# Performance work log

Hardware: AMD Instinct MI355X
Metric: run time of the kernel (lower is better)

The kernel has to match this reference:

```python
import jax, jax.numpy as jnp
import numpy as np

B, L, D, H, NB = 32, 200, 512, 8, 2
HD = D // H
EPS = 1e-8


def _ln(x, g, b):
    m = x.mean(-1, keepdims=True)
    v = ((x - m) ** 2).mean(-1, keepdims=True)
    return (x - m) / jnp.sqrt(v + EPS) * g + b


def setup_inputs() -> dict:
    key = jax.random.key(0)
    ks = jax.random.split(key, 12)
    w = lambda k, shape: (jax.random.normal(k, shape, jnp.float32) * 0.02)
    return {
        "x": jax.random.normal(ks[0], (B, L, D), jnp.float32),
        "timeline_mask": jnp.zeros((B, L), dtype=bool),  # True = padded
        "ln1_g": jnp.ones((NB, D), jnp.float32), "ln1_b": jnp.zeros((NB, D), jnp.float32),
        "Wq": w(ks[1], (NB, D, D)), "bq": jnp.zeros((NB, D), jnp.float32),
        "Wk": w(ks[2], (NB, D, D)), "bk": jnp.zeros((NB, D), jnp.float32),
        "Wv": w(ks[3], (NB, D, D)), "bv": jnp.zeros((NB, D), jnp.float32),
        "Wo": w(ks[4], (NB, D, D)), "bo": jnp.zeros((NB, D), jnp.float32),
        "ln2_g": jnp.ones((NB, D), jnp.float32), "ln2_b": jnp.zeros((NB, D), jnp.float32),
        "W1": w(ks[5], (NB, D, D)), "b1": jnp.zeros((NB, D), jnp.float32),
        "W2": w(ks[6], (NB, D, D)), "b2": jnp.zeros((NB, D), jnp.float32),
        "lnf_g": jnp.ones((D,), jnp.float32), "lnf_b": jnp.zeros((D,), jnp.float32),
    }


def reference(x, timeline_mask, ln1_g, ln1_b, Wq, bq, Wk, bk, Wv, bv, Wo, bo,
              ln2_g, ln2_b, W1, b1, W2, b2, lnf_g, lnf_b):
    valid = (~timeline_mask)[..., None].astype(x.dtype)  # [B,L,1]
    # causal additive bias [L,L]: 0 on/below diag, -inf above
    causal = jnp.where(jnp.tril(jnp.ones((L, L), dtype=bool)), 0.0, -jnp.inf).astype(x.dtype)
    scale = 1.0 / (HD ** 0.5)
    q = x * valid  # dropout = identity (eval)
    for i in range(NB):
        Qn = _ln(q, ln1_g[i], ln1_b[i])  # pre-attn LayerNorm (query side)
        qh = (Qn @ Wq[i] + bq[i]).reshape(B, L, H, HD)
        kh = (q @ Wk[i] + bk[i]).reshape(B, L, H, HD)
        vh = (q @ Wv[i] + bv[i]).reshape(B, L, H, HD)
        scores = jnp.einsum('bqhd,bkhd->bhqk', qh, kh) * scale + causal
        attn = jax.nn.softmax(scores, axis=-1)
        ctx = jnp.einsum('bhqk,bkhd->bqhd', attn, vh).reshape(B, L, D)
        q = ctx @ Wo[i] + bo[i] + Qn          # residual to normed Q (as in source)
        q = _ln(q, ln2_g[i], ln2_b[i])        # forward layernorm
        h = jax.nn.relu(q @ W1[i] + b1[i]) @ W2[i] + b2[i]  # 1x1 convs == per-token MLP
        q = (q + h) * valid                   # PWFF residual, then timeline mask
    return _ln(q, lnf_g, lnf_b)
```

## Files before the change

kernel.cpp:

```cpp
#include <hip/hip_runtime.h>

typedef unsigned short u16;
typedef __bf16 bfloat;
typedef bfloat bf16x8 __attribute__((ext_vector_type(8)));
typedef float f32x4 __attribute__((ext_vector_type(4)));
typedef u16 v8u16 __attribute__((ext_vector_type(8)));
typedef u16 v4u16 __attribute__((ext_vector_type(4)));

#define B_ 32
#define L_ 200
#define D_ 512
#define H_ 8
#define HD_ 64
#define M_ (B_*L_)

__device__ __forceinline__ float bf2f(u16 u) {
  union { float f; unsigned int i; } v; v.i = ((unsigned int)u) << 16; return v.f;
}
__device__ __forceinline__ u16 f2bf(float f) {
  union { float f; unsigned int i; } v; v.f = f;
  unsigned int i = v.i;
  return (u16)((i + 0x7FFFu + ((i >> 16) & 1u)) >> 16);
}
__device__ __forceinline__ bf16x8 as_bf(v8u16 v) { return __builtin_bit_cast(bf16x8, v); }

__device__ __forceinline__ void gload16(const void* g, void* l) {
  __builtin_amdgcn_global_load_lds(
      (const __attribute__((address_space(1))) void*)g,
      (__attribute__((address_space(3))) void*)l,
      16, 0, 0);
}

struct TPtrs { const float* s[12]; };

__global__ __launch_bounds__(256) void prep_kernel(
    const float* __restrict__ x, const unsigned char* __restrict__ mask,
    u16* __restrict__ qb, TPtrs tp, u16* __restrict__ dst)
{
  __shared__ float T[64][65];
  int bid = blockIdx.x;
  int t = threadIdx.x;
  if (bid < 1600) {
    size_t i = (size_t)bid * 256 + t;
    size_t base = i * 8;
    int tok = (int)(base >> 9);
    float valid = mask[tok] ? 0.f : 1.f;
    float4 v0 = *(const float4*)(x + base);
    float4 v1 = *(const float4*)(x + base + 4);
    v8u16 ob;
    ob[0]=f2bf(v0.x*valid); ob[1]=f2bf(v0.y*valid); ob[2]=f2bf(v0.z*valid); ob[3]=f2bf(v0.w*valid);
    ob[4]=f2bf(v1.x*valid); ob[5]=f2bf(v1.y*valid); ob[6]=f2bf(v1.z*valid); ob[7]=f2bf(v1.w*valid);
    *(v8u16*)(qb + base) = ob;
  } else {
    int wb   = bid - 1600;
    int mat  = wb >> 6;
    int tile = wb & 63;
    int tr = tile >> 3, tc = tile & 7;
    const float* src = tp.s[mat];
    #pragma unroll
    for (int i = 0; i < 4; i++) {
      int idx = t + i * 256;
      int row = idx >> 4, c4 = idx & 15;
      float4 v = *(const float4*)(src + (size_t)(tr * 64 + row) * 512 + tc * 64 + c4 * 4);
      T[row][c4 * 4 + 0] = v.x; T[row][c4 * 4 + 1] = v.y;
      T[row][c4 * 4 + 2] = v.z; T[row][c4 * 4 + 3] = v.w;
    }
    __syncthreads();
    u16* d = dst + (size_t)mat * 262144;
    #pragma unroll
    for (int i = 0; i < 2; i++) {
      int idx = t + i * 256;
      int row = idx >> 3, c8 = idx & 7;
      v8u16 v;
      #pragma unroll
      for (int j = 0; j < 8; j++) v[j] = f2bf(T[c8 * 8 + j][row]);
      *(v8u16*)(d + (size_t)(tc * 64 + row) * 512 + tr * 64 + c8 * 8) = v;
    }
  }
}

template<bool OUTF32>
__global__ __launch_bounds__(256) void ln_kernel(
    const u16* __restrict__ in, const float* __restrict__ g, const float* __restrict__ b,
    u16* __restrict__ outb, float* __restrict__ outf)
{
  int row  = blockIdx.x * 4 + (threadIdx.x >> 6);
  int lane = threadIdx.x & 63;
  size_t base = (size_t)row * 512 + lane * 8;
  v8u16 xv = *(const v8u16*)(in + base);
  float xs[8];
  #pragma unroll
  for (int j = 0; j < 8; j++) xs[j] = bf2f(xv[j]);
  float s = 0.f, q = 0.f;
  #pragma unroll
  for (int j = 0; j < 8; j++) { s += xs[j]; q += xs[j] * xs[j]; }
  #pragma unroll
  for (int off = 1; off < 64; off <<= 1) { s += __shfl_xor(s, off); q += __shfl_xor(q, off); }
  float mean = s * (1.f / 512.f);
  float var  = fmaxf(q * (1.f / 512.f) - mean * mean, 0.f);
  float rstd = rsqrtf(var + 1e-8f);
  float4 g0 = *(const float4*)(g + lane * 8);
  float4 g1 = *(const float4*)(g + lane * 8 + 4);
  float4 b0 = *(const float4*)(b + lane * 8);
  float4 b1 = *(const float4*)(b + lane * 8 + 4);
  float gv[8] = {g0.x,g0.y,g0.z,g0.w,g1.x,g1.y,g1.z,g1.w};
  float bv[8] = {b0.x,b0.y,b0.z,b0.w,b1.x,b1.y,b1.z,b1.w};
  if (OUTF32) {
    float of[8];
    #pragma unroll
    for (int j = 0; j < 8; j++) of[j] = (xs[j] - mean) * rstd * gv[j] + bv[j];
    *(float4*)(outf + base)     = make_float4(of[0], of[1], of[2], of[3]);
    *(float4*)(outf + base + 4) = make_float4(of[4], of[5], of[6], of[7]);
  } else {
    v8u16 ob;
    #pragma unroll
    for (int j = 0; j < 8; j++) ob[j] = f2bf((xs[j] - mean) * rstd * gv[j] + bv[j]);
    *(v8u16*)(outb + base) = ob;
  }
}

__device__ __forceinline__ void gemm_core(
    const u16* __restrict__ A, const u16* __restrict__ Wt,
    int m0, int n0, u16* As, u16* Bs, f32x4 (&acc)[2][4])
{
  int tid = threadIdx.x, wid = tid >> 6, lane = tid & 63;
  int wr = wid >> 1, wc = wid & 1;
  int l15 = lane & 15, hi = lane >> 4;
  int sr8 = lane >> 3;
  int gsw = (lane & 7) ^ sr8;

  for (int s = 0; s < 8; s++) {
    int kk = s * 64;
    #pragma unroll
    for (int i = 0; i < 2; i++) {
      int rb = i * 32 + wid * 8;
      gload16(A + (size_t)(m0 + rb + sr8) * 512 + kk + gsw * 8, (char*)As + rb * 128);
    }
    #pragma unroll
    for (int j = 0; j < 4; j++) {
      int rb = j * 32 + wid * 8;
      gload16(Wt + (size_t)(n0 + rb + sr8) * 512 + kk + gsw * 8, (char*)Bs + rb * 128);
    }
    __syncthreads();
    #pragma unroll
    for (int ksub = 0; ksub < 2; ksub++) {
      int ga = ksub * 4 + hi;
      bf16x8 af[2], bfr[4];
      #pragma unroll
      for (int mi = 0; mi < 2; mi++) {
        int ra = wr * 32 + mi * 16 + l15;
        af[mi] = *(const bf16x8*)(As + ra * 64 + ((ga ^ (ra & 7)) * 8));
      }
      #pragma unroll
      for (int ni = 0; ni < 4; ni++) {
        int rb = wc * 64 + ni * 16 + l15;
        bfr[ni] = *(const bf16x8*)(Bs + rb * 64 + ((ga ^ (rb & 7)) * 8));
      }
      #pragma unroll
      for (int mi = 0; mi < 2; mi++)
        #pragma unroll
        for (int ni = 0; ni < 4; ni++)
          acc[mi][ni] = __builtin_amdgcn_mfma_f32_16x16x32_bf16(af[mi], bfr[ni], acc[mi][ni], 0, 0, 0);
    }
    __syncthreads();
  }
}

template<bool RELU, bool HAS_RES, bool MASK>
__global__ __launch_bounds__(256) void gemm_one(
    const u16* __restrict__ A, const u16* __restrict__ Wt, const float* __restrict__ bias,
    const u16* __restrict__ res, const unsigned char* __restrict__ mask,
    u16* __restrict__ outb)
{
  __shared__ u16 As[64 * 64];
  __shared__ u16 Bs[128 * 64];
  int bid = blockIdx.x;
  int m0 = (bid >> 2) * 64, n0 = (bid & 3) * 128;
  f32x4 acc[2][4] = {};
  gemm_core(A, Wt, m0, n0, As, Bs, acc);

  int tid = threadIdx.x, wid = tid >> 6, lane = tid & 63;
  int wr = wid >> 1, wc = wid & 1;
  int l15 = lane & 15, hi = lane >> 4;
  #pragma unroll
  for (int ni = 0; ni < 4; ni++) {
    int gc = n0 + wc * 64 + ni * 16 + l15;
    float bvv = bias[gc];
    #pragma unroll
    for (int mi = 0; mi < 2; mi++) {
      int grb = m0 + wr * 32 + mi * 16 + hi * 4;
      #pragma unroll
      for (int r = 0; r < 4; r++) {
        int gr = grb + r;
        float v = acc[mi][ni][r] + bvv;
        if (HAS_RES) v += bf2f(res[(size_t)gr * 512 + gc]);
        if (RELU) v = fmaxf(v, 0.f);
        if (MASK) v = mask[gr] ? 0.f : v;
        outb[(size_t)gr * 512 + gc] = f2bf(v);
      }
    }
  }
}

__global__ __launch_bounds__(256) void gemm_qkv(
    const u16* __restrict__ Aq, const u16* __restrict__ Akv,
    const u16* __restrict__ Wtq, const u16* __restrict__ Wtk, const u16* __restrict__ Wtv,
    const float* __restrict__ bq, const float* __restrict__ bk, const float* __restrict__ bv,
    u16* __restrict__ outq, u16* __restrict__ outk, u16* __restrict__ outvt)
{
  __shared__ u16 As[64 * 64];
  __shared__ u16 Bs[128 * 64];
  int bid = blockIdx.x;
  int mat = bid / 400;
  int rr = bid - mat * 400;
  int m0 = (rr >> 2) * 64, n0 = (rr & 3) * 128;
  const u16*   A    = (mat == 0) ? Aq  : Akv;
  const u16*   Wt   = (mat == 0) ? Wtq : ((mat == 1) ? Wtk : Wtv);
  const float* bias = (mat == 0) ? bq  : ((mat == 1) ? bk  : bv);
  f32x4 acc[2][4] = {};
  gemm_core(A, Wt, m0, n0, As, Bs, acc);

  int tid = threadIdx.x, wid = tid >> 6, lane = tid & 63;
  int wr = wid >> 1, wc = wid & 1;
  int l15 = lane & 15, hi = lane >> 4;
  if (mat == 2) {
    #pragma unroll
    for (int ni = 0; ni < 4; ni++) {
      int gc = n0 + wc * 64 + ni * 16 + l15;
      float bvv = bias[gc];
      int h = gc >> 6, hd = gc & 63;
      #pragma unroll
      for (int mi = 0; mi < 2; mi++) {
        int grb = m0 + wr * 32 + mi * 16 + hi * 4;
        #pragma unroll
        for (int r = 0; r < 4; r++) {
          int gr = grb + r;
          int b = gr / 200, l = gr - b * 200;
          outvt[((size_t)(b * 8 + h) * 64 + hd) * 224 + l] = f2bf(acc[mi][ni][r] + bvv);
        }
      }
    }
  } else {
    u16* outb = (mat == 0) ? outq : outk;
    #pragma unroll
    for (int ni = 0; ni < 4; ni++) {
      int gc = n0 + wc * 64 + ni * 16 + l15;
      float bvv = bias[gc];
      #pragma unroll
      for (int mi = 0; mi < 2; mi++) {
        int grb = m0 + wr * 32 + mi * 16 + hi * 4;
        #pragma unroll
        for (int r = 0; r < 4; r++) {
          int gr = grb + r;
          outb[(size_t)gr * 512 + gc] = f2bf(acc[mi][ni][r] + bvv);
        }
      }
    }
  }
}

__global__ __launch_bounds__(64) void attn_kernel(
    const u16* __restrict__ Qh, const u16* __restrict__ Kh,
    const u16* __restrict__ Vt, u16* __restrict__ ctx)
{
  __shared__ u16 Pb[2][16 * 32];
  int bid = blockIdx.x;
  int xcd = bid & 7, j = bid >> 3;
  int bh_hi = j / 7, s = j - bh_hi * 7;
  int bh = bh_hi * 8 + xcd;
  int b = bh >> 3, h = bh & 7;
  int lane = threadIdx.x;
  int l15 = lane & 15, hi = lane >> 4;

  const u16* Kg = Kh + (size_t)(b * L_) * D_ + h * HD_;
  const u16* Vg = Vt + (size_t)bh * 64 * 224;

  int tA = (s < 6) ? (12 - s) : 6;
  int tB = (s < 6) ? s : -1;

  for (int jj = 0; jj < 2; jj++) {
    int t = jj ? tB : tA;
    if (t < 0) break;
    int q0 = t * 16;
    int qrow = q0 + l15; if (qrow > L_ - 1) qrow = L_ - 1;
    const u16* Qg = Qh + (size_t)(b * L_ + qrow) * D_ + h * HD_ + hi * 8;
    bf16x8 aq0 = as_bf(*(const v8u16*)(Qg));
    bf16x8 aq1 = as_bf(*(const v8u16*)(Qg + 32));

    f32x4 sv[13];
    float m0[4];
    #pragma unroll
    for (int r = 0; r < 4; r++) m0[r] = -3.0e38f;

    #pragma unroll
    for (int kt = 0; kt < 13; kt++) {
      if (kt <= t) {
        const u16* kp = Kg + (size_t)(kt * 16 + l15) * D_ + hi * 8;
        bf16x8 bk0 = as_bf(*(const v8u16*)(kp));
        bf16x8 bk1 = as_bf(*(const v8u16*)(kp + 32));
        f32x4 a = {0.f, 0.f, 0.f, 0.f};
        a = __builtin_amdgcn_mfma_f32_16x16x32_bf16(aq0, bk0, a, 0, 0, 0);
        a = __builtin_amdgcn_mfma_f32_16x16x32_bf16(aq1, bk1, a, 0, 0, 0);
        #pragma unroll
        for (int r = 0; r < 4; r++) {
          int qr = q0 + hi * 4 + r;
          int kc = kt * 16 + l15;
          float val = (kc <= qr && qr < L_) ? a[r] * 0.125f : -3.0e38f;
          sv[kt][r] = val;
          m0[r] = fmaxf(m0[r], val);
        }
      }
    }
    #pragma unroll
    for (int r = 0; r < 4; r++) {
      #pragma unroll
      for (int off = 1; off < 16; off <<= 1)
        m0[r] = fmaxf(m0[r], __shfl_xor(m0[r], off));
      if (m0[r] < -1e37f) m0[r] = 0.f;
    }
    float sum[4] = {0.f, 0.f, 0.f, 0.f};
    #pragma unroll
    for (int kt = 0; kt < 13; kt++) {
      if (kt <= t) {
        #pragma unroll
        for (int r = 0; r < 4; r++) {
          float p = __expf(sv[kt][r] - m0[r]);
          sv[kt][r] = p;
          sum[r] += p;
        }
      }
    }
    #pragma unroll
    for (int r = 0; r < 4; r++) {
      #pragma unroll
      for (int off = 1; off < 16; off <<= 1) sum[r] += __shfl_xor(sum[r], off);
    }
    float inv[4];
    #pragma unroll
    for (int r = 0; r < 4; r++) inv[r] = sum[r] > 0.f ? 1.f / sum[r] : 0.f;

    int ksmax = (t + 2) >> 1;
    f32x4 acc[4] = {};
    #pragma unroll
    for (int ks = 0; ks < 7; ks++) {
      if (ks < ksmax) {
        u16* Ps = (u16*)Pb[ks & 1];
        #pragma unroll
        for (int half = 0; half < 2; half++) {
          int kt = ks * 2 + half;
          #pragma unroll
          for (int r = 0; r < 4; r++) {
            float pv = (kt <= t) ? sv[kt][r] : 0.f;
            Ps[(hi * 4 + r) * 32 + half * 16 + l15] = f2bf(pv);
          }
        }
        bf16x8 ap = as_bf(*(const v8u16*)(Ps + l15 * 32 + hi * 8));
        #pragma unroll
        for (int nt = 0; nt < 4; nt++) {
          bf16x8 bv = as_bf(*(const v8u16*)(Vg + (nt * 16 + l15) * 224 + ks * 32 + hi * 8));
          acc[nt] = __builtin_amdgcn_mfma_f32_16x16x32_bf16(ap, bv, acc[nt], 0, 0, 0);
        }
      }
    }
    #pragma unroll
    for (int nt = 0; nt < 4; nt++) {
      #pragma unroll
      for (int r = 0; r < 4; r++) {
        int qr = q0 + hi * 4 + r;
        if (qr < L_) ctx[(size_t)(b * L_ + qr) * D_ + h * HD_ + nt * 16 + l15] = f2bf(acc[nt][r] * inv[r]);
      }
    }
  }
}

extern "C" void kernel_launch(void* const* d_in, const int* in_sizes, int n_in,
                              void* d_out, int out_size, void* d_ws, size_t ws_size,
                              hipStream_t stream)
{
  (void)in_sizes; (void)n_in; (void)out_size; (void)ws_size;
  const float* x    = (const float*)d_in[0];
  const unsigned char* mask = (const unsigned char*)d_in[1];
  const float* ln1g = (const float*)d_in[2];
  const float* ln1b = (const float*)d_in[3];
  const float* Wq   = (const float*)d_in[4];
  const float* bq   = (const float*)d_in[5];
  const float* Wk   = (const float*)d_in[6];
  const float* bk   = (const float*)d_in[7];
  const float* Wv   = (const float*)d_in[8];
  const float* bv   = (const float*)d_in[9];
  const float* Wo   = (const float*)d_in[10];
  const float* bo   = (const float*)d_in[11];
  const float* ln2g = (const float*)d_in[12];
  const float* ln2b = (const float*)d_in[13];
  const float* W1   = (const float*)d_in[14];
  const float* b1   = (const float*)d_in[15];
  const float* W2   = (const float*)d_in[16];
  const float* b2   = (const float*)d_in[17];
  const float* lnfg = (const float*)d_in[18];
  const float* lnfb = (const float*)d_in[19];

  char* ws = (char*)d_ws;
  u16* Wt  = (u16*)(ws);
  u16* qb  = (u16*)(ws +  6291456);
  u16* Qn  = (u16*)(ws + 12845056);
  u16* qh  = (u16*)(ws + 19398656);
  u16* kh  = (u16*)(ws + 25952256);
  u16* vh  = (u16*)(ws + 32505856);
  u16* Vtb = (u16*)(ws + 39059456);

  TPtrs tp;
  tp.s[0] = Wq; tp.s[1] = Wq + 262144;
  tp.s[2] = Wk; tp.s[3] = Wk + 262144;
  tp.s[4] = Wv; tp.s[5] = Wv + 262144;
  tp.s[6] = Wo; tp.s[7] = Wo + 262144;
  tp.s[8] = W1; tp.s[9] = W1 + 262144;
  tp.s[10] = W2; tp.s[11] = W2 + 262144;

  prep_kernel<<<dim3(2368), dim3(256), 0, stream>>>(x, mask, qb, tp, Wt);

  for (int i = 0; i < 2; i++) {
    const u16* Wtq = Wt + (size_t)(0 + i) * 262144;
    const u16* Wtk = Wt + (size_t)(2 + i) * 262144;
    const u16* Wtv = Wt + (size_t)(4 + i) * 262144;
    const u16* Wto = Wt + (size_t)(6 + i) * 262144;
    const u16* Wt1 = Wt + (size_t)(8 + i) * 262144;
    const u16* Wt2 = Wt + (size_t)(10 + i) * 262144;

    ln_kernel<false><<<dim3(1600), dim3(256), 0, stream>>>(qb, ln1g + i * 512, ln1b + i * 512, Qn, nullptr);
    gemm_qkv<<<dim3(1200), dim3(256), 0, stream>>>(Qn, qb, Wtq, Wtk, Wtv,
                                                   bq + i * 512, bk + i * 512, bv + i * 512,
                                                   qh, kh, Vtb);
    attn_kernel<<<dim3(1792), dim3(64), 0, stream>>>(qh, kh, Vtb, vh);
    gemm_one<false,true,false><<<dim3(400), dim3(256), 0, stream>>>(vh, Wto, bo + i * 512, Qn, nullptr, qb);
    ln_kernel<false><<<dim3(1600), dim3(256), 0, stream>>>(qb, ln2g + i * 512, ln2b + i * 512, Qn, nullptr);
    gemm_one<true,false,false><<<dim3(400), dim3(256), 0, stream>>>(Qn, Wt1, b1 + i * 512, nullptr, nullptr, qh);
    gemm_one<false,true,true><<<dim3(400), dim3(256), 0, stream>>>(qh, Wt2, b2 + i * 512, Qn, mask, qb);
  }
  ln_kernel<true><<<dim3(1600), dim3(256), 0, stream>>>(qb, lnfg, lnfb, nullptr, (float*)d_out);
}
```

Baseline: 196.3 us.

## Fuse pre-attention and pre-FFN LayerNorms into the following GEMM prologues

The separate LayerNorm kernels before the Q projection and the W1 GEMM are removed. Each GEMM block now loads its full 64x512 A panel into padded LDS, normalizes the rows in place, and writes Qn to global only from the n0==0 block so the residual paths can still read it. Q and K/V projections are split into two launches, and a block-index swizzle is added to all 400-block GEMMs to improve L2 reuse of the weight tiles. In exchange, LDS use per block grows (about 82 KB), which reduces occupancy, and the LayerNorm work is repeated four times per row tile.

Result: slower. 240.4 us (+22.5%).

```diff
diff --git a/kernel.cpp b/kernel.cpp
--- a/kernel.cpp
+++ b/kernel.cpp
@@ -13,6 +13,7 @@
 #define H_ 8
 #define HD_ 64
 #define M_ (B_*L_)
+#define APAD 520
 
 __device__ __forceinline__ float bf2f(u16 u) {
   union { float f; unsigned int i; } v; v.i = ((unsigned int)u) << 16; return v.f;
@@ -79,10 +80,9 @@
   }
 }
 
-template<bool OUTF32>
 __global__ __launch_bounds__(256) void ln_kernel(
     const u16* __restrict__ in, const float* __restrict__ g, const float* __restrict__ b,
-    u16* __restrict__ outb, float* __restrict__ outf)
+    float* __restrict__ outf)
 {
   int row  = blockIdx.x * 4 + (threadIdx.x >> 6);
   int lane = threadIdx.x & 63;
@@ -105,18 +105,11 @@
   float4 b1 = *(const float4*)(b + lane * 8 + 4);
   float gv[8] = {g0.x,g0.y,g0.z,g0.w,g1.x,g1.y,g1.z,g1.w};
   float bv[8] = {b0.x,b0.y,b0.z,b0.w,b1.x,b1.y,b1.z,b1.w};
-  if (OUTF32) {
-    float of[8];
-    #pragma unroll
-    for (int j = 0; j < 8; j++) of[j] = (xs[j] - mean) * rstd * gv[j] + bv[j];
-    *(float4*)(outf + base)     = make_float4(of[0], of[1], of[2], of[3]);
-    *(float4*)(outf + base + 4) = make_float4(of[4], of[5], of[6], of[7]);
-  } else {
-    v8u16 ob;
-    #pragma unroll
-    for (int j = 0; j < 8; j++) ob[j] = f2bf((xs[j] - mean) * rstd * gv[j] + bv[j]);
-    *(v8u16*)(outb + base) = ob;
-  }
+  float of[8];
+  #pragma unroll
+  for (int j = 0; j < 8; j++) of[j] = (xs[j] - mean) * rstd * gv[j] + bv[j];
+  *(float4*)(outf + base)     = make_float4(of[0], of[1], of[2], of[3]);
+  *(float4*)(outf + base + 4) = make_float4(of[4], of[5], of[6], of[7]);
 }
 
 __device__ __forceinline__ void gemm_core(
@@ -164,6 +157,93 @@
     }
     __syncthreads();
   }
+}
+
+__device__ __forceinline__ void gemm_ln_core(
+    const u16* __restrict__ Araw, const u16* __restrict__ Wt,
+    const float* __restrict__ lng, const float* __restrict__ lnb,
+    u16* __restrict__ outQn, bool writeQn,
+    int m0, int n0, u16* Apan, u16* Bs, f32x4 (&acc)[2][4])
+{
+  int tid = threadIdx.x, wid = tid >> 6, lane = tid & 63;
+  int wr = wid >> 1, wc = wid & 1;
+  int l15 = lane & 15, hi = lane >> 4;
+  int sr8 = lane >> 3;
+  int gsw = (lane & 7) ^ sr8;
+
+  #pragma unroll
+  for (int it = 0; it < 16; it++) {
+    int idx = it * 256 + tid;
+    int row = idx >> 6, gg = idx & 63;
+    v8u16 v = *(const v8u16*)(Araw + (size_t)(m0 + row) * 512 + gg * 8);
+    *(v8u16*)(Apan + row * APAD + gg * 8) = v;
+  }
+  __syncthreads();
+
+  for (int i = 0; i < 16; i++) {
+    int r = wid * 16 + i;
+    v8u16 xv = *(const v8u16*)(Apan + r * APAD + lane * 8);
+    float xs[8];
+    #pragma unroll
+    for (int j = 0; j < 8; j++) xs[j] = bf2f(xv[j]);
+    float s = 0.f, q = 0.f;
+    #pragma unroll
+    for (int j = 0; j < 8; j++) { s += xs[j]; q += xs[j] * xs[j]; }
+    #pragma unroll
+    for (int off = 1; off < 64; off <<= 1) { s += __shfl_xor(s, off); q += __shfl_xor(q, off); }
+    float mean = s * (1.f / 512.f);
+    float var  = fmaxf(q * (1.f / 512.f) - mean * mean, 0.f);
+    float rstd = rsqrtf(var + 1e-8f);
+    float4 g0 = *(const float4*)(lng + lane * 8);
+    float4 g1 = *(const float4*)(lng + lane * 8 + 4);
+    float4 b0 = *(const float4*)(lnb + lane * 8);
+    float4 b1 = *(const float4*)(lnb + lane * 8 + 4);
+    float gv[8] = {g0.x,g0.y,g0.z,g0.w,g1.x,g1.y,g1.z,g1.w};
+    float bv[8] = {b0.x,b0.y,b0.z,b0.w,b1.x,b1.y,b1.z,b1.w};
+    v8u16 ob;
+    #pragma unroll
+    for (int j = 0; j < 8; j++) ob[j] = f2bf((xs[j] - mean) * rstd * gv[j] + bv[j]);
+    *(v8u16*)(Apan + r * APAD + lane * 8) = ob;
+    if (writeQn) *(v8u16*)(outQn + (size_t)(m0 + r) * 512 + lane * 8) = ob;
+  }
+  __syncthreads();
+
+  for (int s = 0; s < 8; s++) {
+    int kk = s * 64;
+    #pragma unroll
+    for (int j = 0; j < 4; j++) {
+      int rb = j * 32 + wid * 8;
+      gload16(Wt + (size_t)(n0 + rb + sr8) * 512 + kk + gsw * 8, (char*)Bs + rb * 128);
+    }
+    __syncthreads();
+    #pragma unroll
+    for (int ksub = 0; ksub < 2; ksub++) {
+      int ga = ksub * 4 + hi;
+      bf16x8 af[2], bfr[4];
+      #pragma unroll
+      for (int mi = 0; mi < 2; mi++) {
+        int ra = wr * 32 + mi * 16 + l15;
+        af[mi] = *(const bf16x8*)(Apan + ra * APAD + kk + ksub * 32 + hi * 8);
+      }
+      #pragma unroll
+      for (int ni = 0; ni < 4; ni++) {
+        int rb = wc * 64 + ni * 16 + l15;
+        bfr[ni] = *(const bf16x8*)(Bs + rb * 64 + ((ga ^ (rb & 7)) * 8));
+      }
+      #pragma unroll
+      for (int mi = 0; mi < 2; mi++)
+        #pragma unroll
+        for (int ni = 0; ni < 4; ni++)
+          acc[mi][ni] = __builtin_amdgcn_mfma_f32_16x16x32_bf16(af[mi], bfr[ni], acc[mi][ni], 0, 0, 0);
+    }
+    __syncthreads();
+  }
+}
+
+__device__ __forceinline__ void swz400(int r, int& m0, int& n0, int& rs) {
+  rs = (r & 7) * 50 + (r >> 3);
+  m0 = (rs >> 2) * 64;
+  n0 = (rs & 3) * 128;
 }
 
 template<bool RELU, bool HAS_RES, bool MASK>
@@ -174,8 +254,8 @@
 {
   __shared__ u16 As[64 * 64];
   __shared__ u16 Bs[128 * 64];
-  int bid = blockIdx.x;
-  int m0 = (bid >> 2) * 64, n0 = (bid & 3) * 128;
+  int m0, n0, rs;
+  swz400(blockIdx.x, m0, n0, rs);
   f32x4 acc[2][4] = {};
   gemm_core(A, Wt, m0, n0, As, Bs, acc);
 
@@ -202,28 +282,84 @@
   }
 }
 
-__global__ __launch_bounds__(256) void gemm_qkv(
-    const u16* __restrict__ Aq, const u16* __restrict__ Akv,
-    const u16* __restrict__ Wtq, const u16* __restrict__ Wtk, const u16* __restrict__ Wtv,
-    const float* __restrict__ bq, const float* __restrict__ bk, const float* __restrict__ bv,
-    u16* __restrict__ outq, u16* __restrict__ outk, u16* __restrict__ outvt)
+__global__ __launch_bounds__(256) void gemm_qln(
+    const u16* __restrict__ Araw, const u16* __restrict__ Wt, const float* __restrict__ bias,
+    const float* __restrict__ lng, const float* __restrict__ lnb,
+    u16* __restrict__ outQn, u16* __restrict__ outb)
+{
+  __shared__ u16 sh[64 * APAD + 128 * 64];
+  int m0, n0, rs;
+  swz400(blockIdx.x, m0, n0, rs);
+  f32x4 acc[2][4] = {};
+  gemm_ln_core(Araw, Wt, lng, lnb, outQn, (rs & 3) == 0, m0, n0, sh, sh + 64 * APAD, acc);
+
+  int tid = threadIdx.x, wid = tid >> 6, lane = tid & 63;
+  int wr = wid >> 1, wc = wid & 1;
+  int l15 = lane & 15, hi = lane >> 4;
+  #pragma unroll
+  for (int ni = 0; ni < 4; ni++) {
+    int gc = n0 + wc * 64 + ni * 16 + l15;
+    float bvv = bias[gc];
+    #pragma unroll
+    for (int mi = 0; mi < 2; mi++) {
+      int grb = m0 + wr * 32 + mi * 16 + hi * 4;
+      #pragma unroll
+      for (int r = 0; r < 4; r++)
+        outb[(size_t)(grb + r) * 512 + gc] = f2bf(acc[mi][ni][r] + bvv);
+    }
+  }
+}
+
+__global__ __launch_bounds__(256) void gemm_w1(
+    const u16* __restrict__ Araw, const u16* __restrict__ Wt, const float* __restrict__ bias,
+    const float* __restrict__ lng, const float* __restrict__ lnb,
+    u16* __restrict__ outQn, u16* __restrict__ outb)
+{
+  __shared__ u16 sh[64 * APAD + 128 * 64];
+  int m0, n0, rs;
+  swz400(blockIdx.x, m0, n0, rs);
+  f32x4 acc[2][4] = {};
+  gemm_ln_core(Araw, Wt, lng, lnb, outQn, (rs & 3) == 0, m0, n0, sh, sh + 64 * APAD, acc);
+
+  int tid = threadIdx.x, wid = tid >> 6, lane = tid & 63;
+  int wr = wid >> 1, wc = wid & 1;
+  int l15 = lane & 15, hi = lane >> 4;
+  #pragma unroll
+  for (int ni = 0; ni < 4; ni++) {
+    int gc = n0 + wc * 64 + ni * 16 + l15;
+    float bvv = bias[gc];
+    #pragma unroll
+    for (int mi = 0; mi < 2; mi++) {
+      int grb = m0 + wr * 32 + mi * 16 + hi * 4;
+      #pragma unroll
+      for (int r = 0; r < 4; r++)
+        outb[(size_t)(grb + r) * 512 + gc] = f2bf(fmaxf(acc[mi][ni][r] + bvv, 0.f));
+    }
+  }
+}
+
+__global__ __launch_bounds__(256) void gemm_kv(
+    const u16* __restrict__ A,
+    const u16* __restrict__ Wtk, const u16* __restrict__ Wtv,
+    const float* __restrict__ bk, const float* __restrict__ bv,
+    u16* __restrict__ outk, u16* __restrict__ outvt)
 {
   __shared__ u16 As[64 * 64];
   __shared__ u16 Bs[128 * 64];
   int bid = blockIdx.x;
   int mat = bid / 400;
-  int rr = bid - mat * 400;
-  int m0 = (rr >> 2) * 64, n0 = (rr & 3) * 128;
-  const u16*   A    = (mat == 0) ? Aq  : Akv;
-  const u16*   Wt   = (mat == 0) ? Wtq : ((mat == 1) ? Wtk : Wtv);
-  const float* bias = (mat == 0) ? bq  : ((mat == 1) ? bk  : bv);
+  int r = bid - mat * 400;
+  int m0, n0, rs;
+  swz400(r, m0, n0, rs);
+  const u16*   Wt   = (mat == 0) ? Wtk : Wtv;
+  const float* bias = (mat == 0) ? bk  : bv;
   f32x4 acc[2][4] = {};
   gemm_core(A, Wt, m0, n0, As, Bs, acc);
 
   int tid = threadIdx.x, wid = tid >> 6, lane = tid & 63;
   int wr = wid >> 1, wc = wid & 1;
   int l15 = lane & 15, hi = lane >> 4;
-  if (mat == 2) {
+  if (mat == 1) {
     #pragma unroll
     for (int ni = 0; ni < 4; ni++) {
       int gc = n0 + wc * 64 + ni * 16 + l15;
@@ -233,15 +369,14 @@
       for (int mi = 0; mi < 2; mi++) {
         int grb = m0 + wr * 32 + mi * 16 + hi * 4;
         #pragma unroll
-        for (int r = 0; r < 4; r++) {
-          int gr = grb + r;
+        for (int rr = 0; rr < 4; rr++) {
+          int gr = grb + rr;
           int b = gr / 200, l = gr - b * 200;
-          outvt[((size_t)(b * 8 + h) * 64 + hd) * 224 + l] = f2bf(acc[mi][ni][r] + bvv);
+          outvt[((size_t)(b * 8 + h) * 64 + hd) * 224 + l] = f2bf(acc[mi][ni][rr] + bvv);
         }
       }
     }
   } else {
-    u16* outb = (mat == 0) ? outq : outk;
     #pragma unroll
     for (int ni = 0; ni < 4; ni++) {
       int gc = n0 + wc * 64 + ni * 16 + l15;
@@ -250,10 +385,8 @@
       for (int mi = 0; mi < 2; mi++) {
         int grb = m0 + wr * 32 + mi * 16 + hi * 4;
         #pragma unroll
-        for (int r = 0; r < 4; r++) {
-          int gr = grb + r;
-          outb[(size_t)gr * 512 + gc] = f2bf(acc[mi][ni][r] + bvv);
-        }
+        for (int rr = 0; rr < 4; rr++)
+          outk[(size_t)(grb + rr) * 512 + gc] = f2bf(acc[mi][ni][rr] + bvv);
       }
     }
   }
@@ -426,15 +559,15 @@
     const u16* Wt1 = Wt + (size_t)(8 + i) * 262144;
     const u16* Wt2 = Wt + (size_t)(10 + i) * 262144;
 
-    ln_kernel<false><<<dim3(1600), dim3(256), 0, stream>>>(qb, ln1g + i * 512, ln1b + i * 512, Qn, nullptr);
-    gemm_qkv<<<dim3(1200), dim3(256), 0, stream>>>(Qn, qb, Wtq, Wtk, Wtv,
-                                                   bq + i * 512, bk + i * 512, bv + i * 512,
-                                                   qh, kh, Vtb);
+    gemm_qln<<<dim3(400), dim3(256), 0, stream>>>(qb, Wtq, bq + i * 512,
+                                                  ln1g + i * 512, ln1b + i * 512, Qn, qh);
+    gemm_kv<<<dim3(800), dim3(256), 0, stream>>>(qb, Wtk, Wtv, bk + i * 512, bv + i * 512,
+                                                 kh, Vtb);
     attn_kernel<<<dim3(1792), dim3(64), 0, stream>>>(qh, kh, Vtb, vh);
     gemm_one<false,true,false><<<dim3(400), dim3(256), 0, stream>>>(vh, Wto, bo + i * 512, Qn, nullptr, qb);
-    ln_kernel<false><<<dim3(1600), dim3(256), 0, stream>>>(qb, ln2g + i * 512, ln2b + i * 512, Qn, nullptr);
-    gemm_one<true,false,false><<<dim3(400), dim3(256), 0, stream>>>(Qn, Wt1, b1 + i * 512, nullptr, nullptr, qh);
+    gemm_w1<<<dim3(400), dim3(256), 0, stream>>>(qb, Wt1, b1 + i * 512,
+                                                 ln2g + i * 512, ln2b + i * 512, Qn, qh);
     gemm_one<false,true,true><<<dim3(400), dim3(256), 0, stream>>>(qh, Wt2, b2 + i * 512, Qn, mask, qb);
   }
-  ln_kernel<true><<<dim3(1600), dim3(256), 0, stream>>>(qb, lnfg, lnfb, nullptr, (float*)d_out);
-}
+  ln_kernel<<<dim3(1600), dim3(256), 0, stream>>>(qb, lnfg, lnfb, (float*)d_out);
+}
```
